# Performance work log

Measured on AMD Instinct MI355X. Metric: run time of the kernel, lower is better.

## Reference

```python
import jax, jax.numpy as jnp
import numpy as np

EMBED_DIM = 768
NUM_HEADS = 12
HEAD_DIM = EMBED_DIM // NUM_HEADS
IMG_LEN = 196
TXT_LEN = 1852
SEQ_LEN = IMG_LEN + TXT_LEN
BATCH = 4
NEG = -1e9


def setup_inputs() -> dict:
    key = jax.random.key(0)
    ks = jax.random.split(key, 10)
    s = 1.0 / np.sqrt(EMBED_DIM)
    return {
        "x": jax.random.normal(ks[0], (BATCH, SEQ_LEN, EMBED_DIM), jnp.float32),
        "input_padding_mask": jax.random.randint(ks[1], (BATCH, TXT_LEN), 0, 2, jnp.int32),
        "Wq": jax.random.normal(ks[2], (EMBED_DIM, EMBED_DIM), jnp.float32) * s,
        "bq": jax.random.normal(ks[3], (EMBED_DIM,), jnp.float32) * 0.01,
        "Wk": jax.random.normal(ks[4], (EMBED_DIM, EMBED_DIM), jnp.float32) * s,
        "bk": jax.random.normal(ks[5], (EMBED_DIM,), jnp.float32) * 0.01,
        "Wv": jax.random.normal(ks[6], (EMBED_DIM, EMBED_DIM), jnp.float32) * s,
        "bv": jax.random.normal(ks[7], (EMBED_DIM,), jnp.float32) * 0.01,
        "Wo": jax.random.normal(ks[8], (EMBED_DIM, EMBED_DIM), jnp.float32) * s,
        "bo": jax.random.normal(ks[9], (EMBED_DIM,), jnp.float32) * 0.01,
    }


def _prefix_causal_mask():
    # tril ones, but all rows fully attend to the image prefix columns
    m = jnp.tril(jnp.ones((SEQ_LEN, SEQ_LEN), jnp.float32))
    m = m.at[:, :IMG_LEN].set(1.0)
    return m


def reference(x, input_padding_mask, Wq, bq, Wk, bk, Wv, bv, Wo, bo):
    B, S, E = x.shape
    H, D = NUM_HEADS, HEAD_DIM
    # torch nn.Linear: y = x @ W.T + b, weight shape [out, in]
    q = (x @ Wq.T + bq).reshape(B, S, H, D).transpose(0, 2, 1, 3)  # [B,H,S,D]
    k = (x @ Wk.T + bk).reshape(B, S, H, D).transpose(0, 2, 1, 3)
    v = (x @ Wv.T + bv).reshape(B, S, H, D).transpose(0, 2, 1, 3)

    sims = jnp.einsum("bhqd,bhkd->bhqk", q, k) / jnp.sqrt(jnp.float32(D))
    mask = _prefix_causal_mask()[None, None]  # [1,1,S,S]
    sims = jnp.where(mask == 0, NEG, sims)

    # padding mask over key positions (image prefix always valid)
    full_pad = jnp.concatenate(
        [jnp.ones((B, IMG_LEN), input_padding_mask.dtype), input_padding_mask], axis=1
    )  # [B,S]
    sims = jnp.where(full_pad[:, None, None, :] == 0, NEG, sims)

    attn = jax.nn.softmax(sims, axis=-1)
    out = jnp.einsum("bhqk,bhkd->bhqd", attn, v)
    out = out.transpose(0, 2, 1, 3).reshape(B, S, E)
    return out @ Wo.T + bo
```

## Files before the change

kernel.cpp:

```cpp
#include <hip/hip_runtime.h>

#define B_ 4
#define S_ 2048
#define E_ 768
#define H_ 12
#define D_ 64
#define IMG_ 196
#define TXT_ 1852
#define NEG_ (-1e9f)
#define QSCALE_ 0.18033688f
#define THR2_ 11.5451f
#define EXP2_(x) __builtin_amdgcn_exp2f(x)

typedef __bf16 bf16x8 __attribute__((ext_vector_type(8)));
typedef float f32x4 __attribute__((ext_vector_type(4)));
typedef float f32x16 __attribute__((ext_vector_type(16)));

__device__ __forceinline__ unsigned short f2b(float f) {
    __bf16 h = (__bf16)f;
    return __builtin_bit_cast(unsigned short, h);
}
__device__ __forceinline__ unsigned int pack2(float lo, float hi) {
    return (unsigned int)f2b(lo) | ((unsigned int)f2b(hi) << 16);
}
__device__ __forceinline__ void gload16(const unsigned short* g, unsigned short* l) {
    __builtin_amdgcn_global_load_lds(
        (const __attribute__((address_space(1))) unsigned int*)g,
        (__attribute__((address_space(3))) unsigned int*)l, 16, 0, 0);
}


__global__ __launch_bounds__(256) void cvt_kernel(const float* __restrict__ src,
                                                  unsigned short* __restrict__ dst,
                                                  int n4) {
    int i = blockIdx.x * 256 + threadIdx.x;
    if (i < n4) {
        float4 f = reinterpret_cast<const float4*>(src)[i];
        ushort4 u;
        u.x = f2b(f.x); u.y = f2b(f.y); u.z = f2b(f.z); u.w = f2b(f.w);
        reinterpret_cast<ushort4*>(dst)[i] = u;
    }
}

__global__ __launch_bounds__(256) void cvtw_kernel(
    const float* __restrict__ w0, const float* __restrict__ w1,
    const float* __restrict__ w2, const float* __restrict__ w3,
    unsigned short* __restrict__ d0, unsigned short* __restrict__ d1,
    unsigned short* __restrict__ d2, unsigned short* __restrict__ d3,
    int n4) {
    int i = blockIdx.x * 256 + threadIdx.x;
    if (i >= n4) return;
    int which = blockIdx.y;
    const float* src = (which == 0) ? w0 : (which == 1) ? w1 : (which == 2) ? w2 : w3;
    unsigned short* dst = (which == 0) ? d0 : (which == 1) ? d1 : (which == 2) ? d2 : d3;
    float4 f = reinterpret_cast<const float4*>(src)[i];
    ushort4 u;
    u.x = f2b(f.x); u.y = f2b(f.y); u.z = f2b(f.z); u.w = f2b(f.w);
    reinterpret_cast<ushort4*>(dst)[i] = u;
}

__global__ __launch_bounds__(256) void padneg_kernel(const int* __restrict__ pad,
                                                     float* __restrict__ padneg) {
    int i = blockIdx.x * 256 + threadIdx.x;
    if (i < B_ * S_) {
        int b = i >> 11, s = i & 2047;
        float v = 0.f;
        if (s >= IMG_) v = pad[b * TXT_ + (s - IMG_)] ? 0.f : NEG_;
        padneg[i] = v;
    }
}

__global__ __launch_bounds__(256) void qkv_gemm(
    const unsigned short* __restrict__ xb,
    const unsigned short* __restrict__ wqb,
    const unsigned short* __restrict__ wkb,
    const unsigned short* __restrict__ wvb,
    const float* __restrict__ bq, const float* __restrict__ bk,
    const float* __restrict__ bv,
    unsigned short* __restrict__ qfb, unsigned short* __restrict__ kfb,
    unsigned short* __restrict__ vfb)
{
    __shared__ __align__(16) unsigned short As[128 * 64];
    __shared__ __align__(16) unsigned short Bs[128 * 64];
    const int m0 = blockIdx.x * 128;
    const int n0 = blockIdx.y * 128;
    const int which = n0 / E_;
    const int ncol0 = n0 % E_;
    const unsigned short* W = (which == 0) ? wqb : ((which == 1) ? wkb : wvb);
    const int t = threadIdx.x;
    const int lane = t & 63, wid = t >> 6;
    const int wr = wid >> 1, wc = wid & 1;
    const int c = lane & 15, g = lane >> 4;
    const int srow = lane >> 3;
    const int sslot = (lane & 7) ^ srow;

    f32x4 acc[4][4];
#pragma unroll
    for (int i = 0; i < 4; ++i)
#pragma unroll
        for (int j = 0; j < 4; ++j) acc[i][j] = (f32x4){0.f, 0.f, 0.f, 0.f};

    for (int k0 = 0; k0 < E_; k0 += 64) {
        __syncthreads();
#pragma unroll
        for (int j = 0; j < 8; ++j) {
            int chunk = wid * 8 + j;
            int isB = chunk >> 4;
            int ch = chunk & 15;
            int row = ch * 8 + srow;
            const unsigned short* src =
                (isB ? W + (size_t)(ncol0 + row) * E_
                     : xb + (size_t)(m0 + row) * E_) + k0 + sslot * 8;
            unsigned short* dst = (isB ? Bs : As) + ch * 512;
            gload16(src, dst);
        }
        __syncthreads();

        bf16x8 af[2][4], bfv[2][4];
#pragma unroll
        for (int kk = 0; kk < 2; ++kk) {
#pragma unroll
            for (int fr = 0; fr < 4; ++fr) {
                int row = wr * 64 + fr * 16 + c;
                af[kk][fr] = *reinterpret_cast<const bf16x8*>(
                    &As[row * 64 + (((kk * 4 + g) ^ (row & 7)) * 8)]);
            }
#pragma unroll
            for (int fc = 0; fc < 4; ++fc) {
                int row = wc * 64 + fc * 16 + c;
                bfv[kk][fc] = *reinterpret_cast<const bf16x8*>(
                    &Bs[row * 64 + (((kk * 4 + g) ^ (row & 7)) * 8)]);
            }
        }
#pragma unroll
        for (int kk = 0; kk < 2; ++kk)
#pragma unroll
            for (int fr = 0; fr < 4; ++fr)
#pragma unroll
                for (int fc = 0; fc < 4; ++fc)
                    acc[fr][fc] = __builtin_amdgcn_mfma_f32_16x16x32_bf16(
                        af[kk][fr], bfv[kk][fc], acc[fr][fc], 0, 0, 0);
    }

    const float* bias_ptr = (which == 0) ? bq : ((which == 1) ? bk : bv);
    if (which != 2) {
        unsigned short* dstbuf = (which == 0) ? qfb : kfb;
        const float oscale = (which == 0) ? QSCALE_ : 1.0f;
#pragma unroll
        for (int fc = 0; fc < 4; ++fc) {
            int e = ncol0 + wc * 64 + fc * 16 + c;
            float bias = bias_ptr[e];
            int hd = e >> 6, d = e & 63;
            int dc = d >> 4, hf = (d >> 3) & 1, e8 = d & 7;
#pragma unroll
            for (int fr = 0; fr < 4; ++fr) {
#pragma unroll
                for (int r = 0; r < 4; ++r) {
                    int m = m0 + wr * 64 + fr * 16 + g * 4 + r;
                    int b = m >> 11, s = m & 2047;
                    int bh = b * H_ + hd, t32 = s >> 5, sl = s & 31;
                    size_t off = ((((size_t)bh * 64 + t32) * 4 + dc) * 64
                                  + hf * 32 + sl) * 8 + e8;
                    dstbuf[off] = f2b((acc[fr][fc][r] + bias) * oscale);
                }
            }
        }
    } else {
#pragma unroll
        for (int fc = 0; fc < 4; ++fc) {
            int e = ncol0 + wc * 64 + fc * 16 + c;
            float bias = bias_ptr[e];
            int hd = e >> 6, d = e & 63;
            int vh = d >> 5, dl = d & 31;
#pragma unroll
            for (int fr = 0; fr < 4; ++fr) {
                int m = m0 + wr * 64 + fr * 16 + g * 4;
                int b = m >> 11, s = m & 2047;
                int bh = b * H_ + hd, t32 = s >> 5, ks = s & 31;
                int mm = ks >> 4, hb = (ks >> 3) & 1, e8 = ks & 7;
                size_t off = (((((size_t)bh * 64 + t32) * 2 + mm) * 2 + vh) * 64
                              + hb * 32 + dl) * 8 + e8;
                uint2 pk;
                pk.x = pack2(acc[fr][fc][0] + bias, acc[fr][fc][1] + bias);
                pk.y = pack2(acc[fr][fc][2] + bias, acc[fr][fc][3] + bias);
                *reinterpret_cast<uint2*>(&vfb[off]) = pk;
            }
        }
    }
}

__global__ __launch_bounds__(256) void attn_kernel(
    const unsigned short* __restrict__ qF,
    const unsigned short* __restrict__ kF,
    const unsigned short* __restrict__ vF,
    const float* __restrict__ padneg,
    unsigned short* __restrict__ ob)
{
    __shared__ float exch[3][34 * 64];
    const int flat = blockIdx.x;
    const int xcd = flat & 7, idx = flat >> 3;
    const int bh = xcd * 6 + (idx >> 6);
    const int qt = 63 - (idx & 63);
    const int b = bh / H_, hh = bh % H_;
    const int t = threadIdx.x;
    const int lane = t & 63, w = t >> 6;
    const int h = lane >> 5, ql = lane & 31;
    const int qbase = qt * 32;
    const int q = qbase + ql;
    const float* pn = padneg + b * S_;

    bf16x8 qf[4];
    {
        const unsigned short* qp = qF + ((size_t)(bh * 64 + qt) * 4) * 512 + lane * 8;
#pragma unroll
        for (int dc = 0; dc < 4; ++dc)
            qf[dc] = *reinterpret_cast<const bf16x8*>(qp + dc * 512);
    }

    f32x16 oa0, oa1;
#pragma unroll
    for (int r = 0; r < 16; ++r) { oa0[r] = 0.f; oa1[r] = 0.f; }
    float mr = -3.0e38f, lr = 0.f;

    int kmax = qbase + 32; if (kmax < IMG_) kmax = IMG_;
    const int nt = (kmax + 31) >> 5;
    const int cchunk = (nt + 3) >> 2;
    const int t0w = w * cchunk;
    const int t1w = min(nt, t0w + cchunk);
    const bool hasC = (t1w == nt) && (t0w < t1w);
    const int preEnd = hasC ? (t1w - 1) : t1w;

    const unsigned short* kbase = kF + ((size_t)bh * 64 * 4) * 512 + lane * 8;
    const unsigned short* vbase = vF + ((size_t)bh * 64 * 4) * 512 + lane * 8;

    auto pvstep = [&](const f32x16& p, const bf16x8 (&vf)[4]) {
        unsigned int pka0 = pack2(p[0], p[1]),   pkb0 = pack2(p[2], p[3]);
        unsigned int pka1 = pack2(p[4], p[5]),   pkb1 = pack2(p[6], p[7]);
        unsigned int pka2 = pack2(p[8], p[9]),   pkb2 = pack2(p[10], p[11]);
        unsigned int pka3 = pack2(p[12], p[13]), pkb3 = pack2(p[14], p[15]);
#pragma unroll
        for (int m = 0; m < 2; ++m) {
            unsigned int keep0 = h ? (m ? pka3 : pka1) : (m ? pka2 : pka0);
            unsigned int keep1 = h ? (m ? pkb3 : pkb1) : (m ? pkb2 : pkb0);
            unsigned int send0 = h ? (m ? pka2 : pka0) : (m ? pka3 : pka1);
            unsigned int send1 = h ? (m ? pkb2 : pkb0) : (m ? pkb3 : pkb1);
            unsigned int x0 = (unsigned int)__shfl_xor((int)send0, 32, 64);
            unsigned int x1 = (unsigned int)__shfl_xor((int)send1, 32, 64);
            uint4 fr;
            fr.x = h ? x0 : keep0;
            fr.y = h ? x1 : keep1;
            fr.z = h ? keep0 : x0;
            fr.w = h ? keep1 : x1;
            bf16x8 pb = __builtin_bit_cast(bf16x8, fr);
            oa0 = __builtin_amdgcn_mfma_f32_32x32x16_bf16(vf[2 * m + 0], pb, oa0, 0, 0, 0);
            oa1 = __builtin_amdgcn_mfma_f32_32x32x16_bf16(vf[2 * m + 1], pb, oa1, 0, 0, 0);
        }
    };

    auto loadpna = [&](float* pna, int k0) {
        *reinterpret_cast<float4*>(&pna[0])  = *reinterpret_cast<const float4*>(&pn[k0 + 0  + 4 * h]);
        *reinterpret_cast<float4*>(&pna[4])  = *reinterpret_cast<const float4*>(&pn[k0 + 8  + 4 * h]);
        *reinterpret_cast<float4*>(&pna[8])  = *reinterpret_cast<const float4*>(&pn[k0 + 16 + 4 * h]);
        *reinterpret_cast<float4*>(&pna[12]) = *reinterpret_cast<const float4*>(&pn[k0 + 24 + 4 * h]);
    };

    int kt = t0w;
    for (; kt + 2 <= preEnd; kt += 2) {
        const unsigned short* kpa = kbase + (size_t)kt * 2048;
        bf16x8 ka[4], kb4[4];
#pragma unroll
        for (int dc = 0; dc < 4; ++dc) {
            ka[dc]  = *reinterpret_cast<const bf16x8*>(kpa + dc * 512);
            kb4[dc] = *reinterpret_cast<const bf16x8*>(kpa + 2048 + dc * 512);
        }
        f32x16 sa, sb;
#pragma unroll
        for (int r = 0; r < 16; ++r) { sa[r] = 0.f; sb[r] = 0.f; }
#pragma unroll
        for (int dc = 0; dc < 4; ++dc) {
            sa = __builtin_amdgcn_mfma_f32_32x32x16_bf16(ka[dc],  qf[dc], sa, 0, 0, 0);
            sb = __builtin_amdgcn_mfma_f32_32x32x16_bf16(kb4[dc], qf[dc], sb, 0, 0, 0);
        }
        bf16x8 va[4], vb[4];
        {
            const unsigned short* vpa = vbase + (size_t)kt * 2048;
#pragma unroll
            for (int j = 0; j < 4; ++j) {
                va[j] = *reinterpret_cast<const bf16x8*>(vpa + j * 512);
                vb[j] = *reinterpret_cast<const bf16x8*>(vpa + 2048 + j * 512);
            }
        }
        float pna[16], pnb[16];
        loadpna(pna, kt * 32);
        loadpna(pnb, kt * 32 + 32);
#pragma unroll
        for (int r = 0; r < 16; ++r) {
            sa[r] += pna[r];
            sb[r] += pnb[r];
        }
        float tm = fmaxf(sa[0], sb[0]);
#pragma unroll
        for (int r = 1; r < 16; ++r) tm = fmaxf(tm, fmaxf(sa[r], sb[r]));
        tm = fmaxf(tm, __shfl_xor(tm, 32, 64));
        if (!__all(tm - mr <= THR2_)) {
            float mnew = fmaxf(mr, tm);
            float alpha = EXP2_(mr - mnew);
            mr = mnew; lr *= alpha;
#pragma unroll
            for (int r = 0; r < 16; ++r) { oa0[r] *= alpha; oa1[r] *= alpha; }
        }
#pragma unroll
        for (int r = 0; r < 16; ++r) {
            sa[r] = EXP2_(sa[r] - mr);
            sb[r] = EXP2_(sb[r] - mr);
        }
        float ss = 0.f;
#pragma unroll
        for (int r = 0; r < 16; ++r) ss += sa[r] + sb[r];
        ss += __shfl_xor(ss, 32, 64);
        lr += ss;
        pvstep(sa, va);
        pvstep(sb, vb);
    }

#pragma unroll 1
    for (int pass = (kt < preEnd) ? 0 : 1; pass < (hasC ? 2 : 1); ++pass) {
        const int tile = pass ? (nt - 1) : kt;
        const bool causal = (pass == 1);
        const unsigned short* kp = kbase + (size_t)tile * 2048;
        bf16x8 kf4[4];
#pragma unroll
        for (int dc = 0; dc < 4; ++dc)
            kf4[dc] = *reinterpret_cast<const bf16x8*>(kp + dc * 512);
        f32x16 s;
#pragma unroll
        for (int r = 0; r < 16; ++r) s[r] = 0.f;
#pragma unroll
        for (int dc = 0; dc < 4; ++dc)
            s = __builtin_amdgcn_mfma_f32_32x32x16_bf16(kf4[dc], qf[dc], s, 0, 0, 0);
        bf16x8 vt[4];
        {
            const unsigned short* vp = vbase + (size_t)tile * 2048;
#pragma unroll
            for (int j = 0; j < 4; ++j)
                vt[j] = *reinterpret_cast<const bf16x8*>(vp + j * 512);
        }
        const int k0 = tile * 32;
        float pna[16];
        loadpna(pna, k0);
#pragma unroll
        for (int r = 0; r < 16; ++r) s[r] += pna[r];
        if (causal) {
#pragma unroll
            for (int r = 0; r < 16; ++r) {
                int key = k0 + (r & 3) + 8 * (r >> 2) + 4 * h;
                if (!((key <= q) || (key < IMG_))) s[r] = NEG_;
            }
        }
        float tm = s[0];
#pragma unroll
        for (int r = 1; r < 16; ++r) tm = fmaxf(tm, s[r]);
        tm = fmaxf(tm, __shfl_xor(tm, 32, 64));
        if (!__all(tm - mr <= THR2_)) {
            float mnew = fmaxf(mr, tm);
            float alpha = EXP2_(mr - mnew);
            mr = mnew; lr *= alpha;
#pragma unroll
            for (int r = 0; r < 16; ++r) { oa0[r] *= alpha; oa1[r] *= alpha; }
        }
#pragma unroll
        for (int r = 0; r < 16; ++r) s[r] = EXP2_(s[r] - mr);
        float ss = 0.f;
#pragma unroll
        for (int r = 0; r < 16; ++r) ss += s[r];
        ss += __shfl_xor(ss, 32, 64);
        lr += ss;
        pvstep(s, vt);
    }

    if (w > 0) {
        float* X = exch[w - 1];
#pragma unroll
        for (int r = 0; r < 16; ++r) {
            X[r * 64 + lane] = oa0[r];
            X[(16 + r) * 64 + lane] = oa1[r];
        }
        X[32 * 64 + lane] = mr;
        X[33 * 64 + lane] = lr;
    }
    __syncthreads();
    if (w > 0) return;

    float mAll = mr;
#pragma unroll
    for (int i = 0; i < 3; ++i) mAll = fmaxf(mAll, exch[i][32 * 64 + lane]);
    float w0 = EXP2_(mr - mAll);
    float L = lr * w0;
#pragma unroll
    for (int r = 0; r < 16; ++r) { oa0[r] *= w0; oa1[r] *= w0; }
#pragma unroll
    for (int i = 0; i < 3; ++i) {
        float wi = EXP2_(exch[i][32 * 64 + lane] - mAll);
        L = fmaf(exch[i][33 * 64 + lane], wi, L);
#pragma unroll
        for (int r = 0; r < 16; ++r) {
            oa0[r] = fmaf(exch[i][r * 64 + lane], wi, oa0[r]);
            oa1[r] = fmaf(exch[i][(16 + r) * 64 + lane], wi, oa1[r]);
        }
    }

    float inv = 1.f / L;
    unsigned short* orow = ob + ((size_t)(b * S_ + q)) * E_ + hh * D_;
#pragma unroll
    for (int gg = 0; gg < 4; ++gg) {
        int d0 = gg * 8 + 4 * h;
        uint2 s0, s1;
        s0.x = pack2(oa0[4 * gg] * inv, oa0[4 * gg + 1] * inv);
        s0.y = pack2(oa0[4 * gg + 2] * inv, oa0[4 * gg + 3] * inv);
        s1.x = pack2(oa1[4 * gg] * inv, oa1[4 * gg + 1] * inv);
        s1.y = pack2(oa1[4 * gg + 2] * inv, oa1[4 * gg + 3] * inv);
        *reinterpret_cast<uint2*>(orow + d0) = s0;
        *reinterpret_cast<uint2*>(orow + 32 + d0) = s1;
    }
}

__global__ __launch_bounds__(256) void oproj_gemm(
    const unsigned short* __restrict__ ab,
    const unsigned short* __restrict__ wob,
    const float* __restrict__ bo,
    float* __restrict__ out)
{
    __shared__ __align__(16) unsigned short As[128 * 64];
    __shared__ __align__(16) unsigned short Bs[128 * 64];
    const int m0 = blockIdx.x * 128;
    const int n0 = blockIdx.y * 128;
    const int t = threadIdx.x;
    const int lane = t & 63, wid = t >> 6;
    const int wr = wid >> 1, wc = wid & 1;
    const int c = lane & 15, g = lane >> 4;
    const int srow = lane >> 3;
    const int sslot = (lane & 7) ^ srow;

    f32x4 acc[4][4];
#pragma unroll
    for (int i = 0; i < 4; ++i)
#pragma unroll
        for (int j = 0; j < 4; ++j) acc[i][j] = (f32x4){0.f, 0.f, 0.f, 0.f};

    for (int k0 = 0; k0 < E_; k0 += 64) {
        __syncthreads();
#pragma unroll
        for (int j = 0; j < 8; ++j) {
            int chunk = wid * 8 + j;
            int isB = chunk >> 4;
            int ch = chunk & 15;
            int row = ch * 8 + srow;
            const unsigned short* src =
                (isB ? wob + (size_t)(n0 + row) * E_
                     : ab + (size_t)(m0 + row) * E_) + k0 + sslot * 8;
            unsigned short* dst = (isB ? Bs : As) + ch * 512;
            gload16(src, dst);
        }
        __syncthreads();

        bf16x8 af[2][4], bfv[2][4];
#pragma unroll
        for (int kk = 0; kk < 2; ++kk) {
#pragma unroll
            for (int fr = 0; fr < 4; ++fr) {
                int row = wr * 64 + fr * 16 + c;
                af[kk][fr] = *reinterpret_cast<const bf16x8*>(
                    &As[row * 64 + (((kk * 4 + g) ^ (row & 7)) * 8)]);
            }
#pragma unroll
            for (int fc = 0; fc < 4; ++fc) {
                int row = wc * 64 + fc * 16 + c;
                bfv[kk][fc] = *reinterpret_cast<const bf16x8*>(
                    &Bs[row * 64 + (((kk * 4 + g) ^ (row & 7)) * 8)]);
            }
        }
#pragma unroll
        for (int kk = 0; kk < 2; ++kk)
#pragma unroll
            for (int fr = 0; fr < 4; ++fr)
#pragma unroll
                for (int fc = 0; fc < 4; ++fc)
                    acc[fr][fc] = __builtin_amdgcn_mfma_f32_16x16x32_bf16(
                        af[kk][fr], bfv[kk][fc], acc[fr][fc], 0, 0, 0);
    }

#pragma unroll
    for (int fc = 0; fc < 4; ++fc) {
        int n = n0 + wc * 64 + fc * 16 + c;
        float bias = bo[n];
#pragma unroll
        for (int fr = 0; fr < 4; ++fr)
#pragma unroll
            for (int r = 0; r < 4; ++r) {
                int m = m0 + wr * 64 + fr * 16 + g * 4 + r;
                out[(size_t)m * E_ + n] = acc[fr][fc][r] + bias;
            }
    }
}

extern "C" void kernel_launch(void* const* d_in, const int* in_sizes, int n_in,
                              void* d_out, int out_size, void* d_ws, size_t ws_size,
                              hipStream_t stream) {
    const float* x  = (const float*)d_in[0];
    const int* pad  = (const int*)d_in[1];
    const float* Wq = (const float*)d_in[2];
    const float* bq = (const float*)d_in[3];
    const float* Wk = (const float*)d_in[4];
    const float* bk = (const float*)d_in[5];
    const float* Wv = (const float*)d_in[6];
    const float* bv = (const float*)d_in[7];
    const float* Wo = (const float*)d_in[8];
    const float* bo = (const float*)d_in[9];
    float* out = (float*)d_out;

    const size_t NX = (size_t)B_ * S_ * E_;
    const size_t NW = (size_t)E_ * E_;
    unsigned short* ws = (unsigned short*)d_ws;
    unsigned short* xb  = ws;
    unsigned short* wqb = xb + NX;
    unsigned short* wkb = wqb + NW;
    unsigned short* wvb = wkb + NW;
    unsigned short* wob = wvb + NW;
    unsigned short* qfb = wob + NW;
    unsigned short* kfb = qfb + NX;
    unsigned short* vfb = kfb + NX;
    unsigned short* obuf = vfb + NX;
    float* padneg = (float*)(obuf + NX);

    cvt_kernel<<<(int)(NX / 4 / 256), 256, 0, stream>>>(x, xb, (int)(NX / 4));
    cvtw_kernel<<<dim3((int)(NW / 4 / 256), 4), 256, 0, stream>>>(
        Wq, Wk, Wv, Wo, wqb, wkb, wvb, wob, (int)(NW / 4));
    padneg_kernel<<<(B_ * S_) / 256, 256, 0, stream>>>(pad, padneg);

    qkv_gemm<<<dim3(64, 18), 256, 0, stream>>>(xb, wqb, wkb, wvb, bq, bk, bv,
                                               qfb, kfb, vfb);
    attn_kernel<<<dim3(3072), 256, 0, stream>>>(qfb, kfb, vfb, padneg, obuf);
    oproj_gemm<<<dim3(64, 6), 256, 0, stream>>>(obuf, wob, bo, out);
}
```

Baseline: 151.7 us.

## Prefetch next K tile pair and tree-reduce softmax max/sum in attention loop

```diff
diff --git a/kernel.cpp b/kernel.cpp
--- a/kernel.cpp
+++ b/kernel.cpp
@@ -207,7 +207,7 @@
     const int h = lane >> 5, ql = lane & 31;
     const int qbase = qt * 32;
     const int q = qbase + ql;
-    const float* pn = padneg + b * S_;
+    const float* pn2 = padneg + b * S_ + 4 * h;
 
     bf16x8 qf[4];
     {
@@ -257,22 +257,19 @@
         }
     };
 
-    auto loadpna = [&](float* pna, int k0) {
-        *reinterpret_cast<float4*>(&pna[0])  = *reinterpret_cast<const float4*>(&pn[k0 + 0  + 4 * h]);
-        *reinterpret_cast<float4*>(&pna[4])  = *reinterpret_cast<const float4*>(&pn[k0 + 8  + 4 * h]);
-        *reinterpret_cast<float4*>(&pna[8])  = *reinterpret_cast<const float4*>(&pn[k0 + 16 + 4 * h]);
-        *reinterpret_cast<float4*>(&pna[12]) = *reinterpret_cast<const float4*>(&pn[k0 + 24 + 4 * h]);
-    };
-
     int kt = t0w;
-    for (; kt + 2 <= preEnd; kt += 2) {
-        const unsigned short* kpa = kbase + (size_t)kt * 2048;
-        bf16x8 ka[4], kb4[4];
+    const unsigned short* kpa = kbase + (size_t)kt * 2048;
+    const unsigned short* vpa = vbase + (size_t)kt * 2048;
+    const float* pp = pn2 + kt * 32;
+    bf16x8 ka[4], kb4[4];
+    if (kt + 2 <= preEnd) {
 #pragma unroll
         for (int dc = 0; dc < 4; ++dc) {
             ka[dc]  = *reinterpret_cast<const bf16x8*>(kpa + dc * 512);
             kb4[dc] = *reinterpret_cast<const bf16x8*>(kpa + 2048 + dc * 512);
         }
+    }
+    for (; kt + 2 <= preEnd; kt += 2) {
         f32x16 sa, sb;
 #pragma unroll
         for (int r = 0; r < 16; ++r) { sa[r] = 0.f; sb[r] = 0.f; }
@@ -281,26 +278,40 @@
             sa = __builtin_amdgcn_mfma_f32_32x32x16_bf16(ka[dc],  qf[dc], sa, 0, 0, 0);
             sb = __builtin_amdgcn_mfma_f32_32x32x16_bf16(kb4[dc], qf[dc], sb, 0, 0, 0);
         }
+        if (kt + 4 <= preEnd) {
+#pragma unroll
+            for (int dc = 0; dc < 4; ++dc) {
+                ka[dc]  = *reinterpret_cast<const bf16x8*>(kpa + 4096 + dc * 512);
+                kb4[dc] = *reinterpret_cast<const bf16x8*>(kpa + 6144 + dc * 512);
+            }
+        }
         bf16x8 va[4], vb[4];
-        {
-            const unsigned short* vpa = vbase + (size_t)kt * 2048;
-#pragma unroll
-            for (int j = 0; j < 4; ++j) {
-                va[j] = *reinterpret_cast<const bf16x8*>(vpa + j * 512);
-                vb[j] = *reinterpret_cast<const bf16x8*>(vpa + 2048 + j * 512);
-            }
+#pragma unroll
+        for (int j = 0; j < 4; ++j) {
+            va[j] = *reinterpret_cast<const bf16x8*>(vpa + j * 512);
+            vb[j] = *reinterpret_cast<const bf16x8*>(vpa + 2048 + j * 512);
         }
         float pna[16], pnb[16];
-        loadpna(pna, kt * 32);
-        loadpna(pnb, kt * 32 + 32);
-#pragma unroll
-        for (int r = 0; r < 16; ++r) {
-            sa[r] += pna[r];
-            sb[r] += pnb[r];
-        }
-        float tm = fmaxf(sa[0], sb[0]);
-#pragma unroll
-        for (int r = 1; r < 16; ++r) tm = fmaxf(tm, fmaxf(sa[r], sb[r]));
+#pragma unroll
+        for (int gg = 0; gg < 4; ++gg) {
+            *reinterpret_cast<float4*>(&pna[4 * gg]) =
+                *reinterpret_cast<const float4*>(pp + gg * 8);
+            *reinterpret_cast<float4*>(&pnb[4 * gg]) =
+                *reinterpret_cast<const float4*>(pp + 32 + gg * 8);
+        }
+#pragma unroll
+        for (int r = 0; r < 16; ++r) { sa[r] += pna[r]; sb[r] += pnb[r]; }
+
+        float x0 = fmaxf(fmaxf(sa[0], sa[1]),   fmaxf(sa[2], sa[3]));
+        float x1 = fmaxf(fmaxf(sa[4], sa[5]),   fmaxf(sa[6], sa[7]));
+        float x2 = fmaxf(fmaxf(sa[8], sa[9]),   fmaxf(sa[10], sa[11]));
+        float x3 = fmaxf(fmaxf(sa[12], sa[13]), fmaxf(sa[14], sa[15]));
+        float y0 = fmaxf(fmaxf(sb[0], sb[1]),   fmaxf(sb[2], sb[3]));
+        float y1 = fmaxf(fmaxf(sb[4], sb[5]),   fmaxf(sb[6], sb[7]));
+        float y2 = fmaxf(fmaxf(sb[8], sb[9]),   fmaxf(sb[10], sb[11]));
+        float y3 = fmaxf(fmaxf(sb[12], sb[13]), fmaxf(sb[14], sb[15]));
+        float tm = fmaxf(fmaxf(fmaxf(x0, x1), fmaxf(x2, x3)),
+                         fmaxf(fmaxf(y0, y1), fmaxf(y2, y3)));
         tm = fmaxf(tm, __shfl_xor(tm, 32, 64));
         if (!__all(tm - mr <= THR2_)) {
             float mnew = fmaxf(mr, tm);
@@ -314,13 +325,20 @@
             sa[r] = EXP2_(sa[r] - mr);
             sb[r] = EXP2_(sb[r] - mr);
         }
-        float ss = 0.f;
-#pragma unroll
-        for (int r = 0; r < 16; ++r) ss += sa[r] + sb[r];
+        float u0 = (sa[0] + sa[1]) + (sa[2] + sa[3]);
+        float u1 = (sa[4] + sa[5]) + (sa[6] + sa[7]);
+        float u2 = (sa[8] + sa[9]) + (sa[10] + sa[11]);
+        float u3 = (sa[12] + sa[13]) + (sa[14] + sa[15]);
+        float v0 = (sb[0] + sb[1]) + (sb[2] + sb[3]);
+        float v1 = (sb[4] + sb[5]) + (sb[6] + sb[7]);
+        float v2 = (sb[8] + sb[9]) + (sb[10] + sb[11]);
+        float v3 = (sb[12] + sb[13]) + (sb[14] + sb[15]);
+        float ss = ((u0 + u1) + (u2 + u3)) + ((v0 + v1) + (v2 + v3));
         ss += __shfl_xor(ss, 32, 64);
         lr += ss;
         pvstep(sa, va);
         pvstep(sb, vb);
+        kpa += 4096; vpa += 4096; pp += 64;
     }
 
 #pragma unroll 1
@@ -347,7 +365,10 @@
         }
         const int k0 = tile * 32;
         float pna[16];
-        loadpna(pna, k0);
+#pragma unroll
+        for (int gg = 0; gg < 4; ++gg)
+            *reinterpret_cast<float4*>(&pna[4 * gg]) =
+                *reinterpret_cast<const float4*>(pn2 + k0 + gg * 8);
 #pragma unroll
         for (int r = 0; r < 16; ++r) s[r] += pna[r];
         if (causal) {
@@ -357,9 +378,11 @@
                 if (!((key <= q) || (key < IMG_))) s[r] = NEG_;
             }
         }
-        float tm = s[0];
-#pragma unroll
-        for (int r = 1; r < 16; ++r) tm = fmaxf(tm, s[r]);
+        float x0 = fmaxf(fmaxf(s[0], s[1]),   fmaxf(s[2], s[3]));
+        float x1 = fmaxf(fmaxf(s[4], s[5]),   fmaxf(s[6], s[7]));
+        float x2 = fmaxf(fmaxf(s[8], s[9]),   fmaxf(s[10], s[11]));
+        float x3 = fmaxf(fmaxf(s[12], s[13]), fmaxf(s[14], s[15]));
+        float tm = fmaxf(fmaxf(x0, x1), fmaxf(x2, x3));
         tm = fmaxf(tm, __shfl_xor(tm, 32, 64));
         if (!__all(tm - mr <= THR2_)) {
             float mnew = fmaxf(mr, tm);
@@ -370,9 +393,11 @@
         }
 #pragma unroll
         for (int r = 0; r < 16; ++r) s[r] = EXP2_(s[r] - mr);
-        float ss = 0.f;
-#pragma unroll
-        for (int r = 0; r < 16; ++r) ss += s[r];
+        float u0 = (s[0] + s[1]) + (s[2] + s[3]);
+        float u1 = (s[4] + s[5]) + (s[6] + s[7]);
+        float u2 = (s[8] + s[9]) + (s[10] + s[11]);
+        float u3 = (s[12] + s[13]) + (s[14] + s[15]);
+        float ss = (u0 + u1) + (u2 + u3);
         ss += __shfl_xor(ss, 32, 64);
         lr += ss;
         pvstep(s, vt);
```

After: 180.4 us. +18.9%, slower.
